# Kernel tuning notes

Measured on AMD Instinct MI355X. Metric: run time of the kernel, lower is better.

Reference implementation:

```python
import jax, jax.numpy as jnp
import numpy as np


def setup_inputs() -> dict:
    key = jax.random.key(0)
    k1, k2 = jax.random.split(key)
    B, N1, N2, D = 8, 4096, 4096, 64
    matrix_1 = jax.random.normal(k1, (B, N1, D), dtype=jnp.float32)
    matrix_2 = jax.random.normal(k2, (B, N2, D), dtype=jnp.float32)
    return {"matrix_1": matrix_1, "matrix_2": matrix_2}


def reference(matrix_1, matrix_2):
    # Original: tile [B,N1,1,D] and [B,1,N2,D] to [B,N1,N2,D], multiply, sum over D.
    # Mathematically identical to a batched matmul; avoid materializing the tiled tensor.
    # similarity[b, i, j] = sum_d matrix_1[b, i, d] * matrix_2[b, j, d]
    return jnp.einsum('bnd,bmd->bnm', matrix_1, matrix_2)
```

## Files before the change

kernel.cpp:

```cpp
#include <hip/hip_runtime.h>
#include <hip/hip_bf16.h>

typedef __attribute__((ext_vector_type(8)))  __bf16 bf16x8;
typedef __attribute__((ext_vector_type(16))) float  f32x16;
typedef __attribute__((ext_vector_type(4)))  float  f32x4;


static __device__ inline bf16x8 to_bf16x8(const float4& a, const float4& b) {
    bf16x8 r;
    r[0] = (__bf16)a.x; r[1] = (__bf16)a.y; r[2] = (__bf16)a.z; r[3] = (__bf16)a.w;
    r[4] = (__bf16)b.x; r[5] = (__bf16)b.y; r[6] = (__bf16)b.z; r[7] = (__bf16)b.w;
    return r;
}

__global__ __launch_bounds__(256) void convert_bf16_kernel(
    const float* __restrict__ in, __bf16* __restrict__ out)
{
    const int i = blockIdx.x * 256 + threadIdx.x;
    const float4 v0 = ((const float4*)in)[2 * i];
    const float4 v1 = ((const float4*)in)[2 * i + 1];
    ((bf16x8*)out)[i] = to_bf16x8(v0, v1);
}

__global__ __launch_bounds__(256) void MatrixAttention_76149770158251_kernel(
    const __bf16* __restrict__ A16, const __bf16* __restrict__ B16,
    float* __restrict__ C)
{
    const int N = 4096, D = 64;
    __shared__ float tile[128 * 128];

    const int lane = threadIdx.x & 63;
    const int wid  = threadIdx.x >> 6;
    const int wr   = wid >> 1;
    const int wc   = wid & 1;
    const int bz   = blockIdx.z;

    const int brow = blockIdx.y * 128;
    const int bcol = blockIdx.x * 128;
    const int row0 = brow + wr * 64;
    const int col0 = bcol + wc * 64;

    const __bf16* __restrict__ Ab = A16 + (size_t)bz * N * D;
    const __bf16* __restrict__ Bb = B16 + (size_t)bz * N * D;
    float* __restrict__ Cb        = C   + (size_t)bz * N * N;

    const int lrow  = lane & 31;
    const int khalf = (lane >> 5) * 8;

    f32x16 acc[2][2];
#pragma unroll
    for (int i = 0; i < 2; ++i)
#pragma unroll
        for (int j = 0; j < 2; ++j) acc[i][j] = (f32x16)0.0f;

#pragma unroll
    for (int ks = 0; ks < 4; ++ks) {
        const int k = ks * 16 + khalf;
        bf16x8 af[2], bfr[2];
#pragma unroll
        for (int rb = 0; rb < 2; ++rb)
            af[rb] = *(const bf16x8*)(Ab + (size_t)(row0 + rb * 32 + lrow) * D + k);
#pragma unroll
        for (int cb = 0; cb < 2; ++cb)
            bfr[cb] = *(const bf16x8*)(Bb + (size_t)(col0 + cb * 32 + lrow) * D + k);
#pragma unroll
        for (int rb = 0; rb < 2; ++rb)
#pragma unroll
            for (int cb = 0; cb < 2; ++cb)
                acc[rb][cb] = __builtin_amdgcn_mfma_f32_32x32x16_bf16(
                    af[rb], bfr[cb], acc[rb][cb], 0, 0, 0);
    }

#pragma unroll
    for (int rb = 0; rb < 2; ++rb)
#pragma unroll
        for (int cb = 0; cb < 2; ++cb) {
            const int col   = wc * 64 + cb * 32 + (lane & 31);
            const int rbase = wr * 64 + rb * 32 + 4 * (lane >> 5);
#pragma unroll
            for (int v = 0; v < 16; ++v) {
                const int r = rbase + (v & 3) + 8 * (v >> 2);
                tile[r * 128 + col] = acc[rb][cb][v];
            }
        }

    __syncthreads();

    const f32x4* t4 = (const f32x4*)tile;
    float* Cbase = Cb + (size_t)brow * N + bcol;
#pragma unroll
    for (int it = 0; it < 16; ++it) {
        const int f  = it * 256 + threadIdx.x;
        const int r  = f >> 5;
        const int cq = f & 31;
        __builtin_nontemporal_store(t4[f], (f32x4*)(Cbase + (size_t)r * N + cq * 4));
    }
}

__global__ __launch_bounds__(256) void gemm_f32_kernel(
    const float* __restrict__ A, const float* __restrict__ Bm,
    float* __restrict__ C)
{
    const int N = 4096, D = 64;
    __shared__ float tile[128 * 128];
    const int lane = threadIdx.x & 63;
    const int wid  = threadIdx.x >> 6;
    const int wr   = wid >> 1;
    const int wc   = wid & 1;
    const int bz   = blockIdx.z;
    const int brow = blockIdx.y * 128;
    const int bcol = blockIdx.x * 128;
    const int row0 = brow + wr * 64;
    const int col0 = bcol + wc * 64;
    const float* __restrict__ Ab = A  + (size_t)bz * N * D;
    const float* __restrict__ Bb = Bm + (size_t)bz * N * D;
    float* __restrict__ Cb       = C  + (size_t)bz * N * N;
    const int lrow  = lane & 31;
    const int khalf = (lane >> 5) * 8;
    f32x16 acc[2][2];
#pragma unroll
    for (int i = 0; i < 2; ++i)
#pragma unroll
        for (int j = 0; j < 2; ++j) acc[i][j] = (f32x16)0.0f;
#pragma unroll
    for (int ks = 0; ks < 4; ++ks) {
        const int k = ks * 16 + khalf;
        bf16x8 af[2], bfr[2];
#pragma unroll
        for (int rb = 0; rb < 2; ++rb) {
            const float* p = Ab + (size_t)(row0 + rb * 32 + lrow) * D + k;
            af[rb] = to_bf16x8(*(const float4*)(p), *(const float4*)(p + 4));
        }
#pragma unroll
        for (int cb = 0; cb < 2; ++cb) {
            const float* p = Bb + (size_t)(col0 + cb * 32 + lrow) * D + k;
            bfr[cb] = to_bf16x8(*(const float4*)(p), *(const float4*)(p + 4));
        }
#pragma unroll
        for (int rb = 0; rb < 2; ++rb)
#pragma unroll
            for (int cb = 0; cb < 2; ++cb)
                acc[rb][cb] = __builtin_amdgcn_mfma_f32_32x32x16_bf16(
                    af[rb], bfr[cb], acc[rb][cb], 0, 0, 0);
    }
#pragma unroll
    for (int rb = 0; rb < 2; ++rb)
#pragma unroll
        for (int cb = 0; cb < 2; ++cb) {
            const int col   = wc * 64 + cb * 32 + (lane & 31);
            const int rbase = wr * 64 + rb * 32 + 4 * (lane >> 5);
#pragma unroll
            for (int v = 0; v < 16; ++v) {
                const int r = rbase + (v & 3) + 8 * (v >> 2);
                tile[r * 128 + col] = acc[rb][cb][v];
            }
        }
    __syncthreads();
    const f32x4* t4 = (const f32x4*)tile;
    float* Cbase = Cb + (size_t)brow * N + bcol;
#pragma unroll
    for (int it = 0; it < 16; ++it) {
        const int f  = it * 256 + threadIdx.x;
        const int r  = f >> 5;
        const int cq = f & 31;
        __builtin_nontemporal_store(t4[f], (f32x4*)(Cbase + (size_t)r * N + cq * 4));
    }
}

extern "C" void kernel_launch(void* const* d_in, const int* in_sizes, int n_in,
                              void* d_out, int out_size, void* d_ws, size_t ws_size,
                              hipStream_t stream) {
    const float* m1 = (const float*)d_in[0];
    const float* m2 = (const float*)d_in[1];
    float* out = (float*)d_out;

    const int N = 4096;
    const size_t elems = (size_t)8 * N * 64;
    dim3 grid(N / 128, N / 128, 8);
    dim3 block(256);

    if (ws_size >= 2 * elems * sizeof(__bf16)) {
        __bf16* A16 = (__bf16*)d_ws;
        __bf16* B16 = A16 + elems;
        dim3 cgrid(elems / 8 / 256);
        convert_bf16_kernel<<<cgrid, block, 0, stream>>>(m1, A16);
        convert_bf16_kernel<<<cgrid, block, 0, stream>>>(m2, B16);
        MatrixAttention_76149770158251_kernel<<<grid, block, 0, stream>>>(A16, B16, out);
    } else {
        gemm_f32_kernel<<<grid, block, 0, stream>>>(m1, m2, out);
    }
}
```

Measured before the change: 115.1 us.

## Enlarge GEMM block tile to 256x256 with 1024 threads and staged epilogue

The bf16 MFMA kernel moves from 128x128 tiles with 4 waves to 256x256 tiles with 16 waves per block, so there are fewer blocks. The output is written through a 64x256 LDS buffer in four phases, one wave-row at a time, to keep LDS use at 64KB. A fragments are preloaded for all k steps and the loop order changes so each B fragment is reused across row blocks. The phased epilogue adds extra __syncthreads and serialises the writes, which may reduce overlap in this store-bound kernel.

```diff
diff --git a/kernel.cpp b/kernel.cpp
--- a/kernel.cpp
+++ b/kernel.cpp
@@ -22,21 +22,22 @@
     ((bf16x8*)out)[i] = to_bf16x8(v0, v1);
 }
 
-__global__ __launch_bounds__(256) void MatrixAttention_76149770158251_kernel(
+__global__ __launch_bounds__(1024) void MatrixAttention_76149770158251_kernel(
     const __bf16* __restrict__ A16, const __bf16* __restrict__ B16,
     float* __restrict__ C)
 {
     const int N = 4096, D = 64;
-    __shared__ float tile[128 * 128];
+    __shared__ float tile[64 * 256];
 
-    const int lane = threadIdx.x & 63;
-    const int wid  = threadIdx.x >> 6;
-    const int wr   = wid >> 1;
-    const int wc   = wid & 1;
+    const int tid  = threadIdx.x;
+    const int lane = tid & 63;
+    const int wid  = tid >> 6;
+    const int wr   = wid >> 2;
+    const int wc   = wid & 3;
     const int bz   = blockIdx.z;
 
-    const int brow = blockIdx.y * 128;
-    const int bcol = blockIdx.x * 128;
+    const int brow = blockIdx.y * 256;
+    const int bcol = blockIdx.x * 256;
     const int row0 = brow + wr * 64;
     const int col0 = bcol + wc * 64;
 
@@ -53,47 +54,53 @@
 #pragma unroll
         for (int j = 0; j < 2; ++j) acc[i][j] = (f32x16)0.0f;
 
-#pragma unroll
-    for (int ks = 0; ks < 4; ++ks) {
-        const int k = ks * 16 + khalf;
-        bf16x8 af[2], bfr[2];
-#pragma unroll
-        for (int rb = 0; rb < 2; ++rb)
-            af[rb] = *(const bf16x8*)(Ab + (size_t)(row0 + rb * 32 + lrow) * D + k);
-#pragma unroll
-        for (int cb = 0; cb < 2; ++cb)
-            bfr[cb] = *(const bf16x8*)(Bb + (size_t)(col0 + cb * 32 + lrow) * D + k);
-#pragma unroll
-        for (int rb = 0; rb < 2; ++rb)
-#pragma unroll
-            for (int cb = 0; cb < 2; ++cb)
-                acc[rb][cb] = __builtin_amdgcn_mfma_f32_32x32x16_bf16(
-                    af[rb], bfr[cb], acc[rb][cb], 0, 0, 0);
-    }
-
+    bf16x8 af[2][4];
 #pragma unroll
     for (int rb = 0; rb < 2; ++rb)
 #pragma unroll
-        for (int cb = 0; cb < 2; ++cb) {
-            const int col   = wc * 64 + cb * 32 + (lane & 31);
-            const int rbase = wr * 64 + rb * 32 + 4 * (lane >> 5);
+        for (int ks = 0; ks < 4; ++ks)
+            af[rb][ks] = *(const bf16x8*)(
+                Ab + (size_t)(row0 + rb * 32 + lrow) * D + ks * 16 + khalf);
+
 #pragma unroll
-            for (int v = 0; v < 16; ++v) {
-                const int r = rbase + (v & 3) + 8 * (v >> 2);
-                tile[r * 128 + col] = acc[rb][cb][v];
-            }
+    for (int cb = 0; cb < 2; ++cb)
+#pragma unroll
+        for (int ks = 0; ks < 4; ++ks) {
+            bf16x8 bfr = *(const bf16x8*)(
+                Bb + (size_t)(col0 + cb * 32 + lrow) * D + ks * 16 + khalf);
+#pragma unroll
+            for (int rb = 0; rb < 2; ++rb)
+                acc[rb][cb] = __builtin_amdgcn_mfma_f32_32x32x16_bf16(
+                    af[rb][ks], bfr, acc[rb][cb], 0, 0, 0);
         }
 
-    __syncthreads();
+    for (int p = 0; p < 4; ++p) {
+        if (p) __syncthreads();
+        if (wr == p) {
+#pragma unroll
+            for (int rb = 0; rb < 2; ++rb)
+#pragma unroll
+                for (int cb = 0; cb < 2; ++cb) {
+                    const int col   = wc * 64 + cb * 32 + (lane & 31);
+                    const int rbase = rb * 32 + 4 * (lane >> 5);
+#pragma unroll
+                    for (int v = 0; v < 16; ++v) {
+                        const int r = rbase + (v & 3) + 8 * (v >> 2);
+                        tile[r * 256 + col] = acc[rb][cb][v];
+                    }
+                }
+        }
+        __syncthreads();
 
-    const f32x4* t4 = (const f32x4*)tile;
-    float* Cbase = Cb + (size_t)brow * N + bcol;
+        const f32x4* t4 = (const f32x4*)tile;
+        float* Cbase = Cb + (size_t)(brow + p * 64) * N + bcol;
 #pragma unroll
-    for (int it = 0; it < 16; ++it) {
-        const int f  = it * 256 + threadIdx.x;
-        const int r  = f >> 5;
-        const int cq = f & 31;
-        __builtin_nontemporal_store(t4[f], (f32x4*)(Cbase + (size_t)r * N + cq * 4));
+        for (int it = 0; it < 4; ++it) {
+            const int f = it * 1024 + tid;
+            const int r = f >> 6;
+            const int c = f & 63;
+            __builtin_nontemporal_store(t4[f], (f32x4*)(Cbase + (size_t)r * N + c * 4));
+        }
     }
 }
 
@@ -176,17 +183,17 @@
 
     const int N = 4096;
     const size_t elems = (size_t)8 * N * 64;
-    dim3 grid(N / 128, N / 128, 8);
-    dim3 block(256);
 
     if (ws_size >= 2 * elems * sizeof(__bf16)) {
         __bf16* A16 = (__bf16*)d_ws;
         __bf16* B16 = A16 + elems;
         dim3 cgrid(elems / 8 / 256);
-        convert_bf16_kernel<<<cgrid, block, 0, stream>>>(m1, A16);
-        convert_bf16_kernel<<<cgrid, block, 0, stream>>>(m2, B16);
-        MatrixAttention_76149770158251_kernel<<<grid, block, 0, stream>>>(A16, B16, out);
+        convert_bf16_kernel<<<cgrid, dim3(256), 0, stream>>>(m1, A16);
+        convert_bf16_kernel<<<cgrid, dim3(256), 0, stream>>>(m2, B16);
+        dim3 grid(N / 256, N / 256, 8);
+        MatrixAttention_76149770158251_kernel<<<grid, dim3(1024), 0, stream>>>(A16, B16, out);
     } else {
-        gemm_f32_kernel<<<grid, block, 0, stream>>>(m1, m2, out);
+        dim3 grid(N / 128, N / 128, 8);
+        gemm_f32_kernel<<<grid, dim3(256), 0, stream>>>(m1, m2, out);
     }
 }
```

Result: slower. 137.7 us (+19.6%).
